# Kernel optimization log

Hardware: AMD Instinct MI355X
Metric: run time of the kernel (lower is better)

Reference implementation:

```python
import jax, jax.numpy as jnp
import numpy as np

SHIFT_SIZE = 5
PAD = 2  # shift_size // 2
EPS = 1e-5


def layernorm(x, g, b):
    m = x.mean(-1, keepdims=True)
    v = ((x - m) ** 2).mean(-1, keepdims=True)
    return (x - m) / jnp.sqrt(v + EPS) * g + b


def axial_shift(x, H, W, D, axis):
    # x: (B, N, C) -> torch-style shift along spatial `axis` of (B,C,H,W,D)
    B, N, C = x.shape
    xn = x.transpose(0, 2, 1).reshape(B, C, H, W, D)
    xn = jnp.pad(xn, ((0, 0), (0, 0), (PAD, PAD), (PAD, PAD), (PAD, PAD)))
    cs = -(-C // SHIFT_SIZE)  # torch.chunk uses ceil-sized chunks
    rolled = [
        jnp.roll(xn[:, i * cs:min((i + 1) * cs, C)], s, axis=axis)
        for i, s in enumerate(range(-PAD, PAD + 1))
    ]
    xc = jnp.concatenate(rolled, axis=1)
    xc = xc[:, :, PAD:PAD + H, PAD:PAD + W, PAD:PAD + D]
    return xc.reshape(B, C, H * W * D).transpose(0, 2, 1)


def dwconv3d(x, w, b, H, W, D):
    # x: (B,N,C), w: (C,1,3,3,3) depthwise
    B, N, C = x.shape
    v = x.transpose(0, 2, 1).reshape(B, C, H, W, D)
    y = jax.lax.conv_general_dilated(
        v, w, window_strides=(1, 1, 1), padding=[(1, 1)] * 3,
        dimension_numbers=('NCDHW', 'OIDHW', 'NCDHW'), feature_group_count=C)
    y = y + b[None, :, None, None, None]
    return y.reshape(B, C, N).transpose(0, 2, 1)


def setup_inputs() -> dict:
    key = jax.random.key(0)
    ks = jax.random.split(key, 12)
    C_in, C = 4, 128
    x = jax.random.normal(ks[0], (1, C_in, 96, 96, 96), dtype=jnp.float32)
    p = {
        'x': x,
        'proj_w': jax.random.normal(ks[1], (C, C_in, 3, 3, 3), jnp.float32) * 0.05,
        'proj_b': jnp.zeros((C,), jnp.float32),
        'g0': jnp.ones((C,), jnp.float32), 'b0': jnp.zeros((C,), jnp.float32),
        'g2': jnp.ones((C,), jnp.float32), 'b2': jnp.zeros((C,), jnp.float32),
        'fc1_w': jax.random.normal(ks[2], (C, C), jnp.float32) * 0.02,
        'fc1_b': jnp.zeros((C,), jnp.float32),
        'dw1_w': jax.random.normal(ks[3], (C, 1, 3, 3, 3), jnp.float32) * 0.1,
        'dw1_b': jnp.zeros((C,), jnp.float32),
        'fc2_w': jax.random.normal(ks[4], (C, C), jnp.float32) * 0.02,
        'fc2_b': jnp.zeros((C,), jnp.float32),
        'dw2_w': jax.random.normal(ks[5], (C, 1, 3, 3, 3), jnp.float32) * 0.1,
        'dw2_b': jnp.zeros((C,), jnp.float32),
        'fc3_w': jax.random.normal(ks[6], (C, C), jnp.float32) * 0.02,
        'fc3_b': jnp.zeros((C,), jnp.float32),
        'gn': jnp.ones((C,), jnp.float32), 'bn': jnp.zeros((C,), jnp.float32),
    }
    return p


def reference(x, proj_w, proj_b, g0, b0, g2, b2, fc1_w, fc1_b, dw1_w, dw1_b,
              fc2_w, fc2_b, dw2_w, dw2_b, fc3_w, fc3_b, gn, bn):
    B = x.shape[0]
    # OverlapPatchEmbed: Conv3d(k=3, s=2, p=1)
    v = jax.lax.conv_general_dilated(
        x, proj_w, window_strides=(2, 2, 2), padding=[(1, 1)] * 3,
        dimension_numbers=('NCDHW', 'OIDHW', 'NCDHW'))
    v = v + proj_b[None, :, None, None, None]
    _, C, H, W, D = v.shape
    t = v.reshape(B, C, H * W * D).transpose(0, 2, 1)  # (B,N,C)
    t = layernorm(t, g0, b0)

    # unext_shifted_Block (dropout/droppath in eval -> identity)
    h = layernorm(t, g2, b2)
    h = axial_shift(h, H, W, D, axis=2)
    h = h @ fc1_w.T + fc1_b
    h = dwconv3d(h, dw1_w, dw1_b, H, W, D)
    h = axial_shift(h, H, W, D, axis=3)
    h = h @ fc2_w.T + fc2_b
    h = dwconv3d(h, dw2_w, dw2_b, H, W, D)
    h = axial_shift(h, H, W, D, axis=4)
    h = h @ fc3_w.T + fc3_b
    h = jax.nn.gelu(h, approximate=False)
    t = t + h

    t = layernorm(t, gn, bn)
    out = t.reshape(B, H, W, D, C).transpose(0, 4, 1, 2, 3)
    return out
```

## Files before the change

kernel.cpp:

```cpp
#include <hip/hip_runtime.h>
#include <hip/hip_bf16.h>
#include <math.h>

#define NTOT 110592
#define SD 48
#define SWD 2304

typedef short s16x8 __attribute__((ext_vector_type(8)));
typedef unsigned short u16x8 __attribute__((ext_vector_type(8)));
typedef unsigned short u16x4 __attribute__((ext_vector_type(4)));
typedef float f32x4 __attribute__((ext_vector_type(4)));
typedef unsigned short u16;

__device__ __forceinline__ float bf2f(u16 u) {
    unsigned int x = ((unsigned int)u) << 16;
    float f; __builtin_memcpy(&f, &x, 4); return f;
}
__device__ __forceinline__ u16 f2bf(float f) {
    __hip_bfloat16 h = __float2bfloat16(f);
    u16 u; __builtin_memcpy(&u, &h, 2); return u;
}
__device__ __forceinline__ u16x8 zero8() {
    u16x8 z;
    #pragma unroll
    for (int j = 0; j < 8; ++j) z[j] = 0;
    return z;
}

__device__ __forceinline__ float gelu_f(float x) {
    float y = x * (0.7978845608f + 0.0356774081f * x * x);
    float e = exp2f(y * 2.885390082f);
    return x - x * __builtin_amdgcn_rcpf(e + 1.f);
}

__device__ __forceinline__ u16x8 ld_shift8(const u16* __restrict__ in, int n, int coord,
                                           int STR, int cbase) {
    int g = cbase / 26;
    int split = 26 * (g + 1) - cbase;
    int sh0 = g - 2;
    int cs0 = coord - sh0;
    u16x8 lo = zero8();
    if (cs0 >= 0 && cs0 < SD) lo = *(const u16x8*)&in[(size_t)(n - sh0 * STR) * 128 + cbase];
    if (split >= 8) return lo;
    u16x8 hi = zero8();
    int cs1 = cs0 - 1;
    if (cs1 >= 0 && cs1 < SD) hi = *(const u16x8*)&in[(size_t)(n - (sh0 + 1) * STR) * 128 + cbase];
    u16x8 r;
    #pragma unroll
    for (int j = 0; j < 8; ++j) r[j] = (j < split) ? lo[j] : hi[j];
    return r;
}

__device__ __forceinline__ int dec_tap(int tau) {
    int ti = (tau >= 18 ? 1 : 0) + (tau >= 9 ? 1 : 0);
    int rem = tau - ti * 9;
    int tj = (rem >= 6 ? 1 : 0) + (rem >= 3 ? 1 : 0);
    int tk = rem - tj * 3;
    return ti * 2080 + tj * 416 + tk * 4;
}

__global__ __launch_bounds__(256) void k_prep(
    const float* __restrict__ pw, const float* __restrict__ fc1w,
    const float* __restrict__ fc2w, const float* __restrict__ fc3w,
    const float* __restrict__ dw1w, const float* __restrict__ dw2w,
    u16* __restrict__ wfP, u16* __restrict__ wf1, u16* __restrict__ wf2,
    u16* __restrict__ wf3, float* __restrict__ dwT1, float* __restrict__ dwT2)
{
    int b = blockIdx.x;
    if (b < 32) {
        int which = b >> 3;
        const float* src = (which == 0) ? pw : (which == 1) ? fc1w : (which == 2) ? fc2w : fc3w;
        u16* dst = (which == 0) ? wfP : (which == 1) ? wf1 : (which == 2) ? wf2 : wf3;
        int idx = (b & 7) * 256 + threadIdx.x;
        int lane = idx & 63;
        int s = (idx >> 6) & 3;
        int t = idx >> 8;
        int co = t * 16 + (lane & 15);
        int kb = s * 32 + (lane >> 4) * 8;
        #pragma unroll
        for (int j = 0; j < 8; ++j) {
            int kk = kb + j;
            float v;
            if (which == 0) {
                int tau = kk >> 2, ci = kk & 3;
                v = (tau < 27) ? src[co * 108 + ci * 27 + tau] : 0.f;
            } else {
                v = src[co * 128 + kk];
            }
            dst[idx * 8 + j] = f2bf(v);
        }
    } else {
        int which = (b - 32) / 14;
        int bb = (b - 32) % 14;
        const float* src = which ? dw2w : dw1w;
        float* dst = which ? dwT2 : dwT1;
        int idx = bb * 256 + threadIdx.x;
        if (idx < 27 * 128) {
            int k = idx >> 7;
            int co = idx & 127;
            dst[idx] = src[co * 27 + k];
        }
    }
}

__global__ __launch_bounds__(384) void k_proj_ln(
    const float* __restrict__ x, const u16* __restrict__ wfrag, const float* __restrict__ pb,
    const float* __restrict__ g0, const float* __restrict__ b0,
    const float* __restrict__ g2, const float* __restrict__ b2,
    u16* __restrict__ t_out, u16* __restrict__ h_out)
{
    __shared__ __align__(16) u16 sm[15 * 104 * 4];
    const int tid = threadIdx.x;
    const int blk = blockIdx.x;
    const int n0 = blk * 96;
    const int oi = blk / 24;
    const int oj0 = (blk % 24) * 2;

    const int lane = tid & 63;

    s16x8 wreg[8][4];
    #pragma unroll
    for (int t = 0; t < 8; ++t)
        #pragma unroll
        for (int s = 0; s < 4; ++s)
            wreg[t][s] = *(const s16x8*)&wfrag[((t * 4 + s) * 64 + lane) * 8];

    if (tid < 15) {
        u16x4 z; z[0] = 0; z[1] = 0; z[2] = 0; z[3] = 0;
        *(u16x4*)&sm[(tid * 104 + 0) * 4] = z;
    }
    if (tid < 360) {
        int r = tid / 24;
        int a = tid - r * 24;
        int ti = r / 5, sl = r - ti * 5;
        int iig = 2 * oi + ti - 1;
        int ijg = 2 * oj0 + sl - 1;
        float4 v[4];
        if (iig >= 0 && ijg >= 0) {
            #pragma unroll
            for (int ci = 0; ci < 4; ++ci)
                v[ci] = *(const float4*)&x[(((size_t)ci * 96 + iig) * 96 + ijg) * 96 + 4 * a];
        } else {
            #pragma unroll
            for (int ci = 0; ci < 4; ++ci) v[ci] = make_float4(0.f, 0.f, 0.f, 0.f);
        }
        #pragma unroll
        for (int j = 0; j < 4; ++j) {
            u16x4 w;
            w[0] = f2bf(((const float*)&v[0])[j]);
            w[1] = f2bf(((const float*)&v[1])[j]);
            w[2] = f2bf(((const float*)&v[2])[j]);
            w[3] = f2bf(((const float*)&v[3])[j]);
            *(u16x4*)&sm[(r * 104 + 4 * a + 1 + j) * 4] = w;
        }
    }
    __syncthreads();

    const int wv = tid >> 6;
    const int rb = wv * 16;
    const int colb = lane & 15;
    const int q = lane >> 4;
    const int arow = rb + colb;
    const int ojloc = (arow >= 48) ? 1 : 0;
    const int okk = arow - ojloc * 48;
    const int P = ojloc * 832 + okk * 8;

    int S[4][2];
    #pragma unroll
    for (int s = 0; s < 4; ++s) {
        int t0 = s * 8 + 2 * q;
        S[s][0] = dec_tap(t0);
        S[s][1] = dec_tap(t0 + 1);
    }

    f32x4 acc[8];
    #pragma unroll
    for (int t = 0; t < 8; ++t) {
        float bb = pb[t * 16 + colb];
        acc[t][0] = bb; acc[t][1] = bb; acc[t][2] = bb; acc[t][3] = bb;
    }
    #pragma unroll
    for (int s = 0; s < 4; ++s) {
        u16x4 v0 = *(const u16x4*)&sm[S[s][0] + P];
        u16x4 v1 = *(const u16x4*)&sm[S[s][1] + P];
        if (s == 3) {
            bool z0 = (q >= 2), z1 = (q >= 1);
            #pragma unroll
            for (int e = 0; e < 4; ++e) {
                if (z0) v0[e] = 0;
                if (z1) v1[e] = 0;
            }
        }
        s16x8 a;
        a[0] = (short)v0[0]; a[1] = (short)v0[1]; a[2] = (short)v0[2]; a[3] = (short)v0[3];
        a[4] = (short)v1[0]; a[5] = (short)v1[1]; a[6] = (short)v1[2]; a[7] = (short)v1[3];
        #pragma unroll
        for (int t = 0; t < 8; ++t)
            acc[t] = __builtin_amdgcn_mfma_f32_16x16x32_bf16(a, wreg[t][s], acc[t], 0, 0, 0);
    }

    float s1[4] = {0.f,0.f,0.f,0.f}, s2[4] = {0.f,0.f,0.f,0.f};
    #pragma unroll
    for (int t = 0; t < 8; ++t)
        #pragma unroll
        for (int r4 = 0; r4 < 4; ++r4) {
            float v = acc[t][r4];
            s1[r4] += v; s2[r4] += v * v;
        }
    #pragma unroll
    for (int r4 = 0; r4 < 4; ++r4)
        #pragma unroll
        for (int m = 1; m < 16; m <<= 1) {
            s1[r4] += __shfl_xor(s1[r4], m);
            s2[r4] += __shfl_xor(s2[r4], m);
        }

    float g0v[8], b0v[8], g2v[8], b2v[8];
    #pragma unroll
    for (int t = 0; t < 8; ++t) {
        int c = t * 16 + colb;
        g0v[t] = g0[c]; b0v[t] = b0[c]; g2v[t] = g2[c]; b2v[t] = b2[c];
    }

    float tval[8][4];
    float u1[4] = {0.f,0.f,0.f,0.f}, u2[4] = {0.f,0.f,0.f,0.f};
    #pragma unroll
    for (int r4 = 0; r4 < 4; ++r4) {
        float mean = s1[r4] * (1.f / 128.f);
        float var  = fmaxf(s2[r4] * (1.f / 128.f) - mean * mean, 0.f);
        float rstd = rsqrtf(var + 1e-5f);
        #pragma unroll
        for (int t = 0; t < 8; ++t) {
            float tv = (acc[t][r4] - mean) * rstd * g0v[t] + b0v[t];
            tval[t][r4] = tv;
            u1[r4] += tv; u2[r4] += tv * tv;
        }
    }
    #pragma unroll
    for (int r4 = 0; r4 < 4; ++r4) {
        #pragma unroll
        for (int m = 1; m < 16; m <<= 1) {
            u1[r4] += __shfl_xor(u1[r4], m);
            u2[r4] += __shfl_xor(u2[r4], m);
        }
    }

    #pragma unroll
    for (int r4 = 0; r4 < 4; ++r4) {
        float mean2 = u1[r4] * (1.f / 128.f);
        float var2  = fmaxf(u2[r4] * (1.f / 128.f) - mean2 * mean2, 0.f);
        float rstd2 = rsqrtf(var2 + 1e-5f);
        int row = rb + q * 4 + r4;
        size_t base = (size_t)(n0 + row) * 128;
        #pragma unroll
        for (int t = 0; t < 8; ++t) {
            int col = t * 16 + colb;
            float tv = tval[t][r4];
            t_out[base + col] = f2bf(tv);
            float hv = (tv - mean2) * rstd2 * g2v[t] + b2v[t];
            h_out[base + col] = f2bf(hv);
        }
    }
}

template <int AXIS>
__global__ __launch_bounds__(256) void k_shift_mm(
    const u16* __restrict__ in, const u16* __restrict__ wfrag, const float* __restrict__ bias,
    u16* __restrict__ out)
{
    const int tid = threadIdx.x;
    const int n0 = blockIdx.x * 64;
    const int lane = tid & 63;
    const int wv = tid >> 6;
    const int colb = lane & 15;
    const int q = lane >> 4;

    s16x8 wreg[8][4];
    #pragma unroll
    for (int t = 0; t < 8; ++t)
        #pragma unroll
        for (int s = 0; s < 4; ++s)
            wreg[t][s] = *(const s16x8*)&wfrag[((t * 4 + s) * 64 + lane) * 8];

    const int arow = wv * 16 + colb;
    const int n = n0 + arow;
    const int STR = (AXIS == 0) ? SWD : (AXIS == 1) ? SD : 1;
    const int coord = (AXIS == 0) ? n / SWD : (AXIS == 1) ? (n / SD) % SD : n % SD;

    f32x4 acc[8];
    #pragma unroll
    for (int t = 0; t < 8; ++t) {
        float bb = bias[t * 16 + colb];
        acc[t][0] = bb; acc[t][1] = bb; acc[t][2] = bb; acc[t][3] = bb;
    }
    #pragma unroll
    for (int s = 0; s < 4; ++s) {
        u16x8 av = ld_shift8(in, n, coord, STR, s * 32 + q * 8);
        s16x8 a = *(s16x8*)&av;
        #pragma unroll
        for (int t = 0; t < 8; ++t)
            acc[t] = __builtin_amdgcn_mfma_f32_16x16x32_bf16(a, wreg[t][s], acc[t], 0, 0, 0);
    }
    #pragma unroll
    for (int r4 = 0; r4 < 4; ++r4) {
        int row = wv * 16 + q * 4 + r4;
        size_t base = (size_t)(n0 + row) * 128;
        #pragma unroll
        for (int t = 0; t < 8; ++t)
            out[base + t * 16 + colb] = f2bf(acc[t][r4]);
    }
}

__global__ __launch_bounds__(256, 4) void k_dw(
    const u16* __restrict__ in, const float* __restrict__ wt, const float* __restrict__ b,
    u16* __restrict__ out)
{
    __shared__ __align__(16) float wtl[27 * 128];
    const int tid = threadIdx.x;
    const int cg = tid & 15;
    const int kq = tid >> 4;
    const int k0 = kq * 3;
    const int bid = blockIdx.x;
    const int ij = (bid & 7) * 288 + (bid >> 3);
    const int i = ij / SD;
    const int j = ij - i * SD;
    const int c = cg * 8;

    for (int t = tid; t < 864; t += 256)
        ((float4*)wtl)[t] = ((const float4*)wt)[t];

    const int kclamp0 = (k0 - 1 < 0) ? 0 : (k0 - 1);
    const int kclamp4 = (k0 + 3 > SD - 1) ? (SD - 1) : (k0 + 3);
    const bool k0bad = (k0 - 1 < 0);
    const bool k4bad = (k0 + 3 > SD - 1);

    float acc[3][8];
    {
        float4 ba = *(const float4*)&b[c];
        float4 bb = *(const float4*)&b[c + 4];
        #pragma unroll
        for (int t = 0; t < 3; ++t) {
            acc[t][0] = ba.x; acc[t][1] = ba.y; acc[t][2] = ba.z; acc[t][3] = ba.w;
            acc[t][4] = bb.x; acc[t][5] = bb.y; acc[t][6] = bb.z; acc[t][7] = bb.w;
        }
    }

    bool okt[9];
    const u16* baseptr[9];
    #pragma unroll
    for (int t9 = 0; t9 < 9; ++t9) {
        int di = t9 / 3 - 1, dj = t9 % 3 - 1;
        int ii = i + di, jj = j + dj;
        okt[t9] = ((unsigned)ii < SD) && ((unsigned)jj < SD);
        int iic = (ii < 0) ? 0 : (ii > SD - 1 ? SD - 1 : ii);
        int jjc = (jj < 0) ? 0 : (jj > SD - 1 ? SD - 1 : jj);
        baseptr[t9] = &in[(size_t)((iic * SD + jjc) * SD) * 128 + c];
    }

    u16x8 win[2][5];
    {
        const u16* base = baseptr[0];
        win[0][0] = *(const u16x8*)(base + (size_t)kclamp0 * 128);
        win[0][1] = *(const u16x8*)(base + (size_t)(k0    ) * 128);
        win[0][2] = *(const u16x8*)(base + (size_t)(k0 + 1) * 128);
        win[0][3] = *(const u16x8*)(base + (size_t)(k0 + 2) * 128);
        win[0][4] = *(const u16x8*)(base + (size_t)kclamp4 * 128);
    }
    __syncthreads();

    #pragma unroll
    for (int t9 = 0; t9 < 9; ++t9) {
        const int cur = t9 & 1;
        if (t9 < 8) {
            const u16* base = baseptr[t9 + 1];
            win[cur ^ 1][0] = *(const u16x8*)(base + (size_t)kclamp0 * 128);
            win[cur ^ 1][1] = *(const u16x8*)(base + (size_t)(k0    ) * 128);
            win[cur ^ 1][2] = *(const u16x8*)(base + (size_t)(k0 + 1) * 128);
            win[cur ^ 1][3] = *(const u16x8*)(base + (size_t)(k0 + 2) * 128);
            win[cur ^ 1][4] = *(const u16x8*)(base + (size_t)kclamp4 * 128);
        }
        if (okt[t9]) {
            const int tap0 = t9 * 3;
            float wv[3][8];
            #pragma unroll
            for (int dk = 0; dk < 3; ++dk) {
                float4 wa = *(const float4*)&wtl[(tap0 + dk) * 128 + c];
                float4 wb = *(const float4*)&wtl[(tap0 + dk) * 128 + c + 4];
                wv[dk][0] = wa.x; wv[dk][1] = wa.y; wv[dk][2] = wa.z; wv[dk][3] = wa.w;
                wv[dk][4] = wb.x; wv[dk][5] = wb.y; wv[dk][6] = wb.z; wv[dk][7] = wb.w;
            }
            #pragma unroll
            for (int s = 0; s < 5; ++s) {
                bool bad = (s == 0 && k0bad) || (s == 4 && k4bad);
                float vs[8];
                #pragma unroll
                for (int m = 0; m < 8; ++m)
                    vs[m] = bad ? 0.f : bf2f(win[cur][s][m]);
                #pragma unroll
                for (int t = 0; t < 3; ++t) {
                    int dk = s - t;
                    if (dk >= 0 && dk < 3) {
                        #pragma unroll
                        for (int m = 0; m < 8; ++m)
                            acc[t][m] = fmaf(wv[dk][m], vs[m], acc[t][m]);
                    }
                }
            }
        }
    }
    #pragma unroll
    for (int t = 0; t < 3; ++t) {
        u16x8 o;
        #pragma unroll
        for (int m = 0; m < 8; ++m) o[m] = f2bf(acc[t][m]);
        *(u16x8*)&out[(size_t)((i * SD + j) * SD + k0 + t) * 128 + c] = o;
    }
}

__global__ __launch_bounds__(256) void k_final(
    const u16* __restrict__ in, const u16* __restrict__ wfrag, const float* __restrict__ bias,
    const u16* __restrict__ tin, const float* __restrict__ gn, const float* __restrict__ bn,
    float* __restrict__ out)
{
    const int tid = threadIdx.x;
    const int n0 = blockIdx.x * 64;
    const int lane = tid & 63;
    const int wv = tid >> 6;
    const int colb = lane & 15;
    const int q = lane >> 4;

    const int nn = wv * 16 + colb;
    const int n = n0 + nn;
    const int coord = n % SD;

    u16x4 tq[8];
    #pragma unroll
    for (int ta = 0; ta < 8; ++ta)
        tq[ta] = *(const u16x4*)&tin[(size_t)n * 128 + ta * 16 + q * 4];

    s16x8 wreg[8][4];
    #pragma unroll
    for (int ta = 0; ta < 8; ++ta)
        #pragma unroll
        for (int s = 0; s < 4; ++s)
            wreg[ta][s] = *(const s16x8*)&wfrag[((ta * 4 + s) * 64 + lane) * 8];

    f32x4 acc[8];
    #pragma unroll
    for (int ta = 0; ta < 8; ++ta)
        #pragma unroll
        for (int r4 = 0; r4 < 4; ++r4)
            acc[ta][r4] = bias[ta * 16 + q * 4 + r4];

    #pragma unroll
    for (int s = 0; s < 4; ++s) {
        u16x8 bv = ld_shift8(in, n, coord, 1, s * 32 + q * 8);
        s16x8 b = *(s16x8*)&bv;
        #pragma unroll
        for (int ta = 0; ta < 8; ++ta)
            acc[ta] = __builtin_amdgcn_mfma_f32_16x16x32_bf16(wreg[ta][s], b, acc[ta], 0, 0, 0);
    }

    float val[8][4];
    float s1 = 0.f, s2 = 0.f;
    #pragma unroll
    for (int ta = 0; ta < 8; ++ta)
        #pragma unroll
        for (int r4 = 0; r4 < 4; ++r4) {
            float v = gelu_f(acc[ta][r4]) + bf2f(tq[ta][r4]);
            val[ta][r4] = v;
            s1 += v; s2 += v * v;
        }
    s1 += __shfl_xor(s1, 16); s2 += __shfl_xor(s2, 16);
    s1 += __shfl_xor(s1, 32); s2 += __shfl_xor(s2, 32);
    float mean = s1 * (1.f / 128.f);
    float var  = fmaxf(s2 * (1.f / 128.f) - mean * mean, 0.f);
    float rstd = rsqrtf(var + 1e-5f);

    #pragma unroll
    for (int ta = 0; ta < 8; ++ta)
        #pragma unroll
        for (int r4 = 0; r4 < 4; ++r4) {
            int co = ta * 16 + q * 4 + r4;
            float o = (val[ta][r4] - mean) * rstd * gn[co] + bn[co];
            out[(size_t)co * NTOT + n] = o;
        }
}

extern "C" void kernel_launch(void* const* d_in, const int* in_sizes, int n_in,
                              void* d_out, int out_size, void* d_ws, size_t ws_size,
                              hipStream_t stream)
{
    const float* x    = (const float*)d_in[0];
    const float* pw   = (const float*)d_in[1];
    const float* pb   = (const float*)d_in[2];
    const float* g0   = (const float*)d_in[3];
    const float* b0   = (const float*)d_in[4];
    const float* g2   = (const float*)d_in[5];
    const float* b2   = (const float*)d_in[6];
    const float* fc1w = (const float*)d_in[7];
    const float* fc1b = (const float*)d_in[8];
    const float* dw1w = (const float*)d_in[9];
    const float* dw1b = (const float*)d_in[10];
    const float* fc2w = (const float*)d_in[11];
    const float* fc2b = (const float*)d_in[12];
    const float* dw2w = (const float*)d_in[13];
    const float* dw2b = (const float*)d_in[14];
    const float* fc3w = (const float*)d_in[15];
    const float* fc3b = (const float*)d_in[16];
    const float* gn   = (const float*)d_in[17];
    const float* bn   = (const float*)d_in[18];
    float* out = (float*)d_out;

    u16* tbuf = (u16*)d_ws;
    u16* h1   = tbuf + (size_t)NTOT * 128;
    u16* h2   = h1 + (size_t)NTOT * 128;
    u16* wfP  = h2 + (size_t)NTOT * 128;
    u16* wf1  = wfP + 16384;
    u16* wf2  = wf1 + 16384;
    u16* wf3  = wf2 + 16384;
    float* dwT1 = (float*)(wf3 + 16384);
    float* dwT2 = dwT1 + 27 * 128;

    k_prep<<<60, 256, 0, stream>>>(pw, fc1w, fc2w, fc3w, dw1w, dw2w,
                                   wfP, wf1, wf2, wf3, dwT1, dwT2);

    k_proj_ln<<<NTOT / 96, 384, 0, stream>>>(x, wfP, pb, g0, b0, g2, b2, tbuf, h1);
    k_shift_mm<0><<<NTOT / 64, 256, 0, stream>>>(h1, wf1, fc1b, h2);
    k_dw<<<SWD, 256, 0, stream>>>(h2, dwT1, dw1b, h1);
    k_shift_mm<1><<<NTOT / 64, 256, 0, stream>>>(h1, wf2, fc2b, h2);
    k_dw<<<SWD, 256, 0, stream>>>(h2, dwT2, dw2b, h1);
    k_final<<<NTOT / 64, 256, 0, stream>>>(h1, wf3, fc3b, tbuf, gn, bn, out);
}
```

Before: 164.8 us.

## Stage MFMA weights and residual in LDS, coalesce final transposed output stores

Both the shift-matmul and final kernels now copy the 128x128 bf16 weight fragments into shared memory once per block and load them per k-step, instead of holding 32 fragment registers per lane. This lowers register pressure, which may raise occupancy. The final kernel also stages the residual tile in LDS and writes the channel-major fp32 output through an LDS transpose buffer, so stores are 16-byte vectors along N rather than scattered 4-byte writes. The cost is extra LDS traffic and barriers, plus roughly 49KB of LDS per block in the final kernel, which limits how many blocks fit per CU.

Result: faster. 154.0 us (-6.6%).

```diff
diff --git a/kernel.cpp b/kernel.cpp
--- a/kernel.cpp
+++ b/kernel.cpp
@@ -268,6 +268,7 @@
     const u16* __restrict__ in, const u16* __restrict__ wfrag, const float* __restrict__ bias,
     u16* __restrict__ out)
 {
+    __shared__ __align__(16) u16 wfl[16384];
     const int tid = threadIdx.x;
     const int n0 = blockIdx.x * 64;
     const int lane = tid & 63;
@@ -275,12 +276,8 @@
     const int colb = lane & 15;
     const int q = lane >> 4;
 
-    s16x8 wreg[8][4];
-    #pragma unroll
-    for (int t = 0; t < 8; ++t)
-        #pragma unroll
-        for (int s = 0; s < 4; ++s)
-            wreg[t][s] = *(const s16x8*)&wfrag[((t * 4 + s) * 64 + lane) * 8];
+    for (int i = tid; i < 2048; i += 256)
+        *(u16x8*)&wfl[i * 8] = *(const u16x8*)&wfrag[i * 8];
 
     const int arow = wv * 16 + colb;
     const int n = n0 + arow;
@@ -293,13 +290,18 @@
         float bb = bias[t * 16 + colb];
         acc[t][0] = bb; acc[t][1] = bb; acc[t][2] = bb; acc[t][3] = bb;
     }
+    __syncthreads();
     #pragma unroll
     for (int s = 0; s < 4; ++s) {
         u16x8 av = ld_shift8(in, n, coord, STR, s * 32 + q * 8);
         s16x8 a = *(s16x8*)&av;
+        s16x8 bf[8];
         #pragma unroll
         for (int t = 0; t < 8; ++t)
-            acc[t] = __builtin_amdgcn_mfma_f32_16x16x32_bf16(a, wreg[t][s], acc[t], 0, 0, 0);
+            bf[t] = *(const s16x8*)&wfl[((t * 4 + s) * 64 + lane) * 8];
+        #pragma unroll
+        for (int t = 0; t < 8; ++t)
+            acc[t] = __builtin_amdgcn_mfma_f32_16x16x32_bf16(a, bf[t], acc[t], 0, 0, 0);
     }
     #pragma unroll
     for (int r4 = 0; r4 < 4; ++r4) {
@@ -422,6 +424,10 @@
     const u16* __restrict__ tin, const float* __restrict__ gn, const float* __restrict__ bn,
     float* __restrict__ out)
 {
+    __shared__ __align__(16) unsigned char smem[50176];
+    u16* wfl = (u16*)smem;
+    u16* T = (u16*)(smem + 32768);
+    float* Osm = (float*)smem;
     const int tid = threadIdx.x;
     const int n0 = blockIdx.x * 64;
     const int lane = tid & 63;
@@ -429,46 +435,47 @@
     const int colb = lane & 15;
     const int q = lane >> 4;
 
+    for (int i = tid; i < 2048; i += 256)
+        *(u16x8*)&wfl[i * 8] = *(const u16x8*)&wfrag[i * 8];
+    for (int i = tid; i < 1024; i += 256) {
+        int row = i >> 4;
+        int c8 = (i & 15) * 8;
+        *(u16x8*)&T[row * 136 + c8] = *(const u16x8*)&tin[(size_t)(n0 + row) * 128 + c8];
+    }
+
     const int nn = wv * 16 + colb;
     const int n = n0 + nn;
     const int coord = n % SD;
 
-    u16x4 tq[8];
-    #pragma unroll
-    for (int ta = 0; ta < 8; ++ta)
-        tq[ta] = *(const u16x4*)&tin[(size_t)n * 128 + ta * 16 + q * 4];
-
-    s16x8 wreg[8][4];
-    #pragma unroll
-    for (int ta = 0; ta < 8; ++ta)
-        #pragma unroll
-        for (int s = 0; s < 4; ++s)
-            wreg[ta][s] = *(const s16x8*)&wfrag[((ta * 4 + s) * 64 + lane) * 8];
-
     f32x4 acc[8];
     #pragma unroll
     for (int ta = 0; ta < 8; ++ta)
         #pragma unroll
         for (int r4 = 0; r4 < 4; ++r4)
             acc[ta][r4] = bias[ta * 16 + q * 4 + r4];
+    __syncthreads();
 
     #pragma unroll
     for (int s = 0; s < 4; ++s) {
         u16x8 bv = ld_shift8(in, n, coord, 1, s * 32 + q * 8);
         s16x8 b = *(s16x8*)&bv;
+        s16x8 af[8];
         #pragma unroll
         for (int ta = 0; ta < 8; ++ta)
-            acc[ta] = __builtin_amdgcn_mfma_f32_16x16x32_bf16(wreg[ta][s], b, acc[ta], 0, 0, 0);
-    }
-
-    float val[8][4];
+            af[ta] = *(const s16x8*)&wfl[((ta * 4 + s) * 64 + lane) * 8];
+        #pragma unroll
+        for (int ta = 0; ta < 8; ++ta)
+            acc[ta] = __builtin_amdgcn_mfma_f32_16x16x32_bf16(af[ta], b, acc[ta], 0, 0, 0);
+    }
+
     float s1 = 0.f, s2 = 0.f;
     #pragma unroll
     for (int ta = 0; ta < 8; ++ta)
         #pragma unroll
         for (int r4 = 0; r4 < 4; ++r4) {
-            float v = gelu_f(acc[ta][r4]) + bf2f(tq[ta][r4]);
-            val[ta][r4] = v;
+            int co = ta * 16 + q * 4 + r4;
+            float v = gelu_f(acc[ta][r4]) + bf2f(T[nn * 136 + co]);
+            acc[ta][r4] = v;
             s1 += v; s2 += v * v;
         }
     s1 += __shfl_xor(s1, 16); s2 += __shfl_xor(s2, 16);
@@ -477,14 +484,26 @@
     float var  = fmaxf(s2 * (1.f / 128.f) - mean * mean, 0.f);
     float rstd = rsqrtf(var + 1e-5f);
 
+    __syncthreads();
+
     #pragma unroll
     for (int ta = 0; ta < 8; ++ta)
         #pragma unroll
         for (int r4 = 0; r4 < 4; ++r4) {
             int co = ta * 16 + q * 4 + r4;
-            float o = (val[ta][r4] - mean) * rstd * gn[co] + bn[co];
-            out[(size_t)co * NTOT + n] = o;
-        }
+            float o = (acc[ta][r4] - mean) * rstd * gn[co] + bn[co];
+            Osm[co * 68 + nn] = o;
+        }
+    __syncthreads();
+
+    #pragma unroll
+    for (int it = 0; it < 8; ++it) {
+        int idx = it * 256 + tid;
+        int row = idx >> 4;
+        int c4 = idx & 15;
+        f32x4 v = *(const f32x4*)&Osm[row * 68 + c4 * 4];
+        *(f32x4*)&out[(size_t)row * NTOT + n0 + c4 * 4] = v;
+    }
 }
 
 extern "C" void kernel_launch(void* const* d_in, const int* in_sizes, int n_in,
```
